# Optimization experiments

Measured on AMD Instinct MI355X. Metric: run time of the kernel, lower is better.

The kernel has to match this reference:

```python
import jax, jax.numpy as jnp
import numpy as np
from jax import lax

DIM = 128
N_CODEBOOKS = 8
CODEBOOK_SIZE = 2048
BATCH = 16
TOKENS = 2048


def setup_inputs() -> dict:
    key = jax.random.key(0)
    k1, k2 = jax.random.split(key)
    x = jax.random.normal(k1, (BATCH, DIM, TOKENS), dtype=jnp.float32)
    # matches nn.Parameter(torch.randn(K, D) / D**0.5) per stage, stacked
    codebooks = jax.random.normal(k2, (N_CODEBOOKS, CODEBOOK_SIZE, DIM),
                                  dtype=jnp.float32) / jnp.sqrt(jnp.float32(DIM))
    return {"x": x, "codebooks": codebooks}


def reference(x, codebooks):
    """Residual VQ forward.

    x: (B, D, T), codebooks: (n_cb, K, D)
    Returns (total_quantized (B,D,T), codes (B,n_cb,T) int32, commitment_loss scalar)
    """
    xt = jnp.transpose(x, (0, 2, 1))  # (B, T, D)

    def step(carry, cb):
        residual, total = carry  # (B,T,D) each; cb: (K,D)
        # squared euclidean distances: ||r||^2 - 2 r.c + ||c||^2 -> (B,T,K)
        dist = (jnp.sum(residual * residual, axis=-1, keepdims=True)
                - 2.0 * jnp.einsum('btd,kd->btk', residual, cb)
                + jnp.sum(cb * cb, axis=-1))
        idx = jnp.argmin(dist, axis=-1)          # (B, T)
        quantized = cb[idx]                       # gather -> (B, T, D)
        # straight-through combine
        q_st = residual + lax.stop_gradient(quantized - residual)
        total = total + q_st
        residual = residual - lax.stop_gradient(quantized)
        # F.mse_loss(residual.detach(), zeros) == mean(residual**2), detached
        loss = jnp.mean(lax.stop_gradient(residual) ** 2)
        return (residual, total), (idx.astype(jnp.int32), loss)

    init = (xt, jnp.zeros_like(xt))
    (_, total), (codes, losses) = lax.scan(step, init, codebooks)
    total_quantized = jnp.transpose(total, (0, 2, 1))   # (B, D, T)
    codes = jnp.transpose(codes, (1, 0, 2))             # (B, n_cb, T)
    commitment_loss = jnp.sum(losses)
    return total_quantized, codes, commitment_loss
```

## Files before the change

### kernel.cpp

```cpp
#include <hip/hip_runtime.h>

#define DIM 128
#define NCB 8
#define KSZ 2048
#define BATCH 16
#define TOK 2048
#define NTOK (BATCH * TOK)
#define NELEM (BATCH * DIM * TOK)
#define T_TILE 128
#define NTHR 512
#define CHUNK 64
#define NCHUNK (KSZ / CHUNK)

typedef float f32x4 __attribute__((ext_vector_type(4)));
typedef short s16x8 __attribute__((ext_vector_type(8)));

__device__ __forceinline__ unsigned short f2bf(float f) {
    unsigned u = __float_as_uint(f);
    u = (u + 0x7FFFu + ((u >> 16) & 1u)) >> 16;
    return (unsigned short)u;
}
__device__ __forceinline__ float bf2f(unsigned short h) {
    return __uint_as_float(((unsigned)h) << 16);
}

__global__ void rvq_prep_hi(const float* __restrict__ cbs,
                            unsigned short* __restrict__ ch) {
    int i = blockIdx.x * 256 + threadIdx.x;
    ch[i] = f2bf(cbs[i]);
}

__global__ void rvq_cnorm(const float* __restrict__ cbs,
                          float* __restrict__ cnorm,
                          float* __restrict__ loss_acc) {
    if (blockIdx.x == 0 && threadIdx.x == 0) *loss_acc = 0.0f;
    int k = blockIdx.x * 256 + threadIdx.x;
    const float4* row = (const float4*)(cbs + (size_t)k * DIM);
    float s = 0.0f;
#pragma unroll
    for (int i = 0; i < DIM / 4; ++i) {
        float4 v = row[i];
        s += v.x * v.x + v.y * v.y + v.z * v.z + v.w * v.w;
    }
    cnorm[k] = s;
}

__global__ __launch_bounds__(NTHR, 2) void rvq_fused(
        const float* __restrict__ x,
        const float* __restrict__ cbs,
        const unsigned short* __restrict__ ch,
        const float* __restrict__ cng,
        float* __restrict__ out,
        float* __restrict__ codes,
        float* __restrict__ loss_acc) {
    __shared__ float res_lds[T_TILE][DIM + 4];
    __shared__ unsigned short Bbuf[2][8192];
    __shared__ float mv1[T_TILE * 16];
    __shared__ int   mi1[T_TILE * 16];
    __shared__ float mv2[T_TILE * 16];
    __shared__ int   mi2[T_TILE * 16];
    __shared__ int   best4s[T_TILE][4];

    const int tid   = threadIdx.x;
    const int lane  = tid & 63;
    const int wv    = __builtin_amdgcn_readfirstlane(tid >> 6);
    const int col16 = lane & 15;
    const int quad  = lane >> 4;

    const int token0 = blockIdx.x * T_TILE;
    const int b      = token0 >> 11;
    const int t_in_b = token0 & (TOK - 1);

    {
        const float* xb = x + (size_t)b * DIM * TOK + t_in_b;
#pragma unroll
        for (int it = 0; it < 8; ++it) {
            int idx = it * NTHR + tid;
            int d  = idx >> 5;
            int t4 = (idx & 31) * 4;
            float4 v = *(const float4*)(xb + (size_t)d * TOK + t4);
            res_lds[t4 + 0][d] = v.x;
            res_lds[t4 + 1][d] = v.y;
            res_lds[t4 + 2][d] = v.z;
            res_lds[t4 + 3][d] = v.w;
        }
    }
    __syncthreads();

    float my_loss = 0.0f;

#define STAGE_PREFETCH(cc)                                                     \
    {                                                                          \
        int _f0 = wv * 2, _f1 = wv * 2 + 1;                                    \
        stg0 = *(const s16x8*)(ch_s +                                          \
            ((size_t)((cc) * CHUNK + (_f0 >> 2) * 16 + col16)) * DIM +         \
            ((_f0 & 3) * 32 + quad * 8));                                      \
        stg1 = *(const s16x8*)(ch_s +                                          \
            ((size_t)((cc) * CHUNK + (_f1 >> 2) * 16 + col16)) * DIM +         \
            ((_f1 & 3) * 32 + quad * 8));                                      \
    }

#define STAGE_WRITE(buf)                                                       \
    {                                                                          \
        *(s16x8*)&Bbuf[buf][(wv * 2) * 512 + lane * 8]     = stg0;             \
        *(s16x8*)&Bbuf[buf][(wv * 2 + 1) * 512 + lane * 8] = stg1;             \
    }

#define COMPUTE(accv, buf)                                                     \
    {                                                                          \
        _Pragma("unroll")                                                      \
        for (int nt = 0; nt < 4; ++nt) accv[nt] = (f32x4){0.f, 0.f, 0.f, 0.f}; \
        _Pragma("unroll")                                                      \
        for (int dc = 0; dc < 4; ++dc) {                                       \
            s16x8 bh0 = *(const s16x8*)&Bbuf[buf][(0 + dc) * 512 + lane * 8];  \
            s16x8 bh1 = *(const s16x8*)&Bbuf[buf][(4 + dc) * 512 + lane * 8];  \
            s16x8 bh2 = *(const s16x8*)&Bbuf[buf][(8 + dc) * 512 + lane * 8];  \
            s16x8 bh3 = *(const s16x8*)&Bbuf[buf][(12 + dc) * 512 + lane * 8]; \
            accv[0] = __builtin_amdgcn_mfma_f32_16x16x32_bf16(ah[dc], bh0, accv[0], 0, 0, 0); \
            accv[1] = __builtin_amdgcn_mfma_f32_16x16x32_bf16(ah[dc], bh1, accv[1], 0, 0, 0); \
            accv[2] = __builtin_amdgcn_mfma_f32_16x16x32_bf16(ah[dc], bh2, accv[2], 0, 0, 0); \
            accv[3] = __builtin_amdgcn_mfma_f32_16x16x32_bf16(ah[dc], bh3, accv[3], 0, 0, 0); \
            accv[0] = __builtin_amdgcn_mfma_f32_16x16x32_bf16(al[dc], bh0, accv[0], 0, 0, 0); \
            accv[1] = __builtin_amdgcn_mfma_f32_16x16x32_bf16(al[dc], bh1, accv[1], 0, 0, 0); \
            accv[2] = __builtin_amdgcn_mfma_f32_16x16x32_bf16(al[dc], bh2, accv[2], 0, 0, 0); \
            accv[3] = __builtin_amdgcn_mfma_f32_16x16x32_bf16(al[dc], bh3, accv[3], 0, 0, 0); \
        }                                                                      \
    }

#define FOLD(accv, cc)                                                         \
    {                                                                          \
        int _ib0 = (cc) * CHUNK + col16;                                       \
        float _cn0 = cn_s[_ib0], _cn1 = cn_s[_ib0 + 16];                       \
        float _cn2 = cn_s[_ib0 + 32], _cn3 = cn_s[_ib0 + 48];                  \
        _Pragma("unroll")                                                      \
        for (int r = 0; r < 4; ++r) {                                          \
            float p0 = fmaf(-2.0f, accv[0][r], _cn0);                          \
            float p1 = fmaf(-2.0f, accv[1][r], _cn1);                          \
            float p2 = fmaf(-2.0f, accv[2][r], _cn2);                          \
            float p3 = fmaf(-2.0f, accv[3][r], _cn3);                          \
            bool c01 = p1 < p0;                                                \
            float m01 = c01 ? p1 : p0; int j01 = c01 ? _ib0 + 16 : _ib0;       \
            bool c23 = p3 < p2;                                                \
            float m23 = c23 ? p3 : p2; int j23 = c23 ? _ib0 + 48 : _ib0 + 32;  \
            bool cf = m23 < m01;                                               \
            float m = cf ? m23 : m01; int jm = cf ? j23 : j01;                 \
            bool b1 = m < v1[r];                                               \
            bool b2 = m < v2[r];                                               \
            v2[r] = b1 ? v1[r] : (b2 ? m : v2[r]);                             \
            i2[r] = b1 ? i1[r] : (b2 ? jm : i2[r]);                            \
            v1[r] = b1 ? m : v1[r];                                            \
            i1[r] = b1 ? jm : i1[r];                                           \
        }                                                                      \
    }

#pragma unroll 1
    for (int s = 0; s < NCB; ++s) {
        const unsigned short* __restrict__ ch_s = ch  + (size_t)s * KSZ * DIM;
        const float* __restrict__ cb_s = cbs + (size_t)s * KSZ * DIM;
        const float* __restrict__ cn_s = cng + (size_t)s * KSZ;

        s16x8 ah[4], al[4];
#pragma unroll
        for (int dc = 0; dc < 4; ++dc) {
            int t  = wv * 16 + col16;
            int d0 = dc * 32 + quad * 8;
            float4 u = *(const float4*)&res_lds[t][d0];
            float4 w = *(const float4*)&res_lds[t][d0 + 4];
            float e[8] = {u.x, u.y, u.z, u.w, w.x, w.y, w.z, w.w};
            s16x8 hv, lv;
#pragma unroll
            for (int j = 0; j < 8; ++j) {
                unsigned short h = f2bf(e[j]);
                hv[j] = (short)h;
                lv[j] = (short)f2bf(e[j] - bf2f(h));
            }
            ah[dc] = hv;
            al[dc] = lv;
        }

        float v1[4], v2[4]; int i1[4], i2[4];
#pragma unroll
        for (int r = 0; r < 4; ++r) {
            v1[r] = 3.4e38f; v2[r] = 3.4e38f; i1[r] = 0; i2[r] = 0;
        }

        s16x8 stg0, stg1;
        f32x4 accA[4], accB[4];

        STAGE_PREFETCH(0); STAGE_WRITE(0); __syncthreads();
        STAGE_PREFETCH(1);
        COMPUTE(accA, 0);
        STAGE_WRITE(1); __syncthreads();
#pragma unroll 1
        for (int c = 1; c < 31; c += 2) {
            STAGE_PREFETCH(c + 1);
            COMPUTE(accB, 1);
            FOLD(accA, c - 1);
            STAGE_WRITE(0);
            __syncthreads();
            STAGE_PREFETCH(c + 2);
            COMPUTE(accA, 0);
            FOLD(accB, c);
            STAGE_WRITE(1);
            __syncthreads();
        }
        COMPUTE(accB, 1);
        FOLD(accA, 30);
        FOLD(accB, 31);

#pragma unroll
        for (int r = 0; r < 4; ++r) {
            int t = wv * 16 + quad * 4 + r;
            mv1[t * 16 + col16] = v1[r];
            mi1[t * 16 + col16] = i1[r];
            mv2[t * 16 + col16] = v2[r];
            mi2[t * 16 + col16] = i2[r];
        }
        __syncthreads();

        if (tid < T_TILE) {
            const int t = tid;
            float bv[4] = {3.4e38f, 3.4e38f, 3.4e38f, 3.4e38f};
            int   bi[4] = {0x7FFFFFFF, 0x7FFFFFFF, 0x7FFFFFFF, 0x7FFFFFFF};
#pragma unroll
            for (int col = 0; col < 16; ++col) {
#pragma unroll
                for (int w = 0; w < 2; ++w) {
                    float v = w ? mv2[t * 16 + col] : mv1[t * 16 + col];
                    int   i = w ? mi2[t * 16 + col] : mi1[t * 16 + col];
#pragma unroll
                    for (int j = 0; j < 4; ++j) {
                        if (v < bv[j] || (v == bv[j] && i < bi[j])) {
                            float tv = bv[j]; bv[j] = v; v = tv;
                            int   ti = bi[j]; bi[j] = i; i = ti;
                        }
                    }
                }
            }
#pragma unroll
            for (int j = 0; j < 4; ++j) best4s[t][j] = bi[j];
        }
        __syncthreads();

        {
            const int t  = tid >> 2;
            const int cs = tid & 3;
            const int cand = best4s[t][cs];
            const float* crow = cb_s + (size_t)cand * DIM;
            float n0 = 0, n1 = 0, n2 = 0, n3 = 0;
            float a0 = 0, a1 = 0, a2 = 0, a3 = 0;
#pragma unroll 8
            for (int d4 = 0; d4 < DIM / 4; ++d4) {
                float4 r4 = *(const float4*)&res_lds[t][d4 * 4];
                float4 q4 = *(const float4*)&crow[d4 * 4];
                n0 = fmaf(r4.x, r4.x, n0); n1 = fmaf(r4.y, r4.y, n1);
                n2 = fmaf(r4.z, r4.z, n2); n3 = fmaf(r4.w, r4.w, n3);
                a0 = fmaf(r4.x, q4.x, a0); a1 = fmaf(r4.y, q4.y, a1);
                a2 = fmaf(r4.z, q4.z, a2); a3 = fmaf(r4.w, q4.w, a3);
            }
            float rn  = (n0 + n1) + (n2 + n3);
            float dot = (a0 + a1) + (a2 + a3);
            float dist = fmaf(-2.0f, dot, rn) + cn_s[cand];
            int best = cand;
#pragma unroll
            for (int mk = 1; mk <= 2; mk <<= 1) {
                float od = __shfl_xor(dist, mk, 64);
                int   oi = __shfl_xor(best, mk, 64);
                if (od < dist || (od == dist && oi < best)) {
                    dist = od; best = oi;
                }
            }
            if (cs == 0)
                codes[(size_t)b * (NCB * TOK) + (size_t)s * TOK + t_in_b + t] =
                    (float)best;
            const float* qrow = cb_s + (size_t)best * DIM;
            float lp = 0.0f;
#pragma unroll
            for (int d4 = 0; d4 < 8; ++d4) {
                int d = cs * 32 + d4 * 4;
                float4 r4 = *(const float4*)&res_lds[t][d];
                float4 q4 = *(const float4*)&qrow[d];
                float4 nr;
                nr.x = r4.x - q4.x; nr.y = r4.y - q4.y;
                nr.z = r4.z - q4.z; nr.w = r4.w - q4.w;
                *(float4*)&res_lds[t][d] = nr;
                lp += nr.x * nr.x + nr.y * nr.y + nr.z * nr.z + nr.w * nr.w;
            }
            my_loss += lp;
        }
        __syncthreads();
    }

    {
        const float* xb = x + (size_t)b * DIM * TOK + t_in_b;
        float* ob = out + (size_t)b * DIM * TOK + t_in_b;
#pragma unroll
        for (int it = 0; it < 8; ++it) {
            int idx = it * NTHR + tid;
            int d  = idx >> 5;
            int t4 = (idx & 31) * 4;
            float4 v = *(const float4*)(xb + (size_t)d * TOK + t4);
            float4 o;
            o.x = v.x - res_lds[t4 + 0][d];
            o.y = v.y - res_lds[t4 + 1][d];
            o.z = v.z - res_lds[t4 + 2][d];
            o.w = v.w - res_lds[t4 + 3][d];
            *(float4*)(ob + (size_t)d * TOK + t4) = o;
        }
    }

#pragma unroll
    for (int off = 32; off > 0; off >>= 1)
        my_loss += __shfl_down(my_loss, off, 64);
    if (lane == 0) atomicAdd(loss_acc, my_loss);
}

__global__ void rvq_loss_fin(const float* __restrict__ loss_acc,
                             float* __restrict__ loss_out) {
    *loss_out = *loss_acc * (1.0f / (float)NELEM);
}

extern "C" void kernel_launch(void* const* d_in, const int* in_sizes, int n_in,
                              void* d_out, int out_size, void* d_ws, size_t ws_size,
                              hipStream_t stream) {
    const float* x   = (const float*)d_in[0];
    const float* cbs = (const float*)d_in[1];

    float* out      = (float*)d_out;
    float* codes    = out + NELEM;
    float* loss_out = out + NELEM + (size_t)BATCH * NCB * TOK;

    float* wsf      = (float*)d_ws;
    float* loss_acc = wsf;
    unsigned short* ch = (unsigned short*)(wsf + 256);
    float* cng = (float*)(ch + (size_t)NCB * KSZ * DIM);

    hipLaunchKernelGGL(rvq_prep_hi, dim3((NCB * KSZ * DIM) / 256), dim3(256),
                       0, stream, cbs, ch);
    hipLaunchKernelGGL(rvq_cnorm, dim3((NCB * KSZ) / 256), dim3(256), 0, stream,
                       cbs, cng, loss_acc);
    hipLaunchKernelGGL(rvq_fused, dim3(NTOK / T_TILE), dim3(NTHR), 0, stream,
                       x, cbs, ch, cng, out, codes, loss_acc);
    hipLaunchKernelGGL(rvq_loss_fin, dim3(1), dim3(1), 0, stream,
                       loss_acc, loss_out);
}
```

Measured before the change: 547.0 us.

## Halve token tile and parallelize top-4 candidate merge across threads with shuffles

Shrinks the token tile to 64 with 256 threads per block, so each wave stages four codebook fragments per chunk and the grid has twice as many blocks. The serial top-4 merge run by one thread per token is replaced by four threads per token, each merging eight candidates and then combining via xor-shuffles. This removes one barrier and the best4s LDS array. Index arrays become 16-bit and the residual row padding changes, cutting LDS use so more blocks can be resident, at the cost of re-streaming the codebook per smaller tile and possible bank-conflict changes.

```diff
diff --git a/kernel.cpp b/kernel.cpp
--- a/kernel.cpp
+++ b/kernel.cpp
@@ -7,8 +7,8 @@
 #define TOK 2048
 #define NTOK (BATCH * TOK)
 #define NELEM (BATCH * DIM * TOK)
-#define T_TILE 128
-#define NTHR 512
+#define T_TILE 64
+#define NTHR 256
 #define CHUNK 64
 #define NCHUNK (KSZ / CHUNK)
 
@@ -53,13 +53,12 @@
         float* __restrict__ out,
         float* __restrict__ codes,
         float* __restrict__ loss_acc) {
-    __shared__ float res_lds[T_TILE][DIM + 4];
+    __shared__ float res_lds[T_TILE][DIM + 2];
     __shared__ unsigned short Bbuf[2][8192];
     __shared__ float mv1[T_TILE * 16];
-    __shared__ int   mi1[T_TILE * 16];
     __shared__ float mv2[T_TILE * 16];
-    __shared__ int   mi2[T_TILE * 16];
-    __shared__ int   best4s[T_TILE][4];
+    __shared__ unsigned short mi1[T_TILE * 16];
+    __shared__ unsigned short mi2[T_TILE * 16];
 
     const int tid   = threadIdx.x;
     const int lane  = tid & 63;
@@ -76,8 +75,8 @@
 #pragma unroll
         for (int it = 0; it < 8; ++it) {
             int idx = it * NTHR + tid;
-            int d  = idx >> 5;
-            int t4 = (idx & 31) * 4;
+            int d  = idx >> 4;
+            int t4 = (idx & 15) * 4;
             float4 v = *(const float4*)(xb + (size_t)d * TOK + t4);
             res_lds[t4 + 0][d] = v.x;
             res_lds[t4 + 1][d] = v.y;
@@ -91,19 +90,20 @@
 
 #define STAGE_PREFETCH(cc)                                                     \
     {                                                                          \
-        int _f0 = wv * 2, _f1 = wv * 2 + 1;                                    \
-        stg0 = *(const s16x8*)(ch_s +                                          \
-            ((size_t)((cc) * CHUNK + (_f0 >> 2) * 16 + col16)) * DIM +         \
-            ((_f0 & 3) * 32 + quad * 8));                                      \
-        stg1 = *(const s16x8*)(ch_s +                                          \
-            ((size_t)((cc) * CHUNK + (_f1 >> 2) * 16 + col16)) * DIM +         \
-            ((_f1 & 3) * 32 + quad * 8));                                      \
+        const unsigned short* _p = ch_s +                                      \
+            ((size_t)((cc) * CHUNK + wv * 16 + col16)) * DIM + quad * 8;       \
+        stg0 = *(const s16x8*)(_p + 0);                                        \
+        stg1 = *(const s16x8*)(_p + 32);                                       \
+        stg2 = *(const s16x8*)(_p + 64);                                       \
+        stg3 = *(const s16x8*)(_p + 96);                                       \
     }
 
 #define STAGE_WRITE(buf)                                                       \
     {                                                                          \
-        *(s16x8*)&Bbuf[buf][(wv * 2) * 512 + lane * 8]     = stg0;             \
-        *(s16x8*)&Bbuf[buf][(wv * 2 + 1) * 512 + lane * 8] = stg1;             \
+        *(s16x8*)&Bbuf[buf][(wv * 4 + 0) * 512 + lane * 8] = stg0;             \
+        *(s16x8*)&Bbuf[buf][(wv * 4 + 1) * 512 + lane * 8] = stg1;             \
+        *(s16x8*)&Bbuf[buf][(wv * 4 + 2) * 512 + lane * 8] = stg2;             \
+        *(s16x8*)&Bbuf[buf][(wv * 4 + 3) * 512 + lane * 8] = stg3;             \
     }
 
 #define COMPUTE(accv, buf)                                                     \
@@ -184,7 +184,7 @@
             v1[r] = 3.4e38f; v2[r] = 3.4e38f; i1[r] = 0; i2[r] = 0;
         }
 
-        s16x8 stg0, stg1;
+        s16x8 stg0, stg1, stg2, stg3;
         f32x4 accA[4], accB[4];
 
         STAGE_PREFETCH(0); STAGE_WRITE(0); __syncthreads();
@@ -212,22 +212,47 @@
         for (int r = 0; r < 4; ++r) {
             int t = wv * 16 + quad * 4 + r;
             mv1[t * 16 + col16] = v1[r];
-            mi1[t * 16 + col16] = i1[r];
+            mi1[t * 16 + col16] = (unsigned short)i1[r];
             mv2[t * 16 + col16] = v2[r];
-            mi2[t * 16 + col16] = i2[r];
+            mi2[t * 16 + col16] = (unsigned short)i2[r];
         }
         __syncthreads();
 
-        if (tid < T_TILE) {
-            const int t = tid;
-            float bv[4] = {3.4e38f, 3.4e38f, 3.4e38f, 3.4e38f};
-            int   bi[4] = {0x7FFFFFFF, 0x7FFFFFFF, 0x7FFFFFFF, 0x7FFFFFFF};
-#pragma unroll
-            for (int col = 0; col < 16; ++col) {
-#pragma unroll
-                for (int w = 0; w < 2; ++w) {
-                    float v = w ? mv2[t * 16 + col] : mv1[t * 16 + col];
-                    int   i = w ? mi2[t * 16 + col] : mi1[t * 16 + col];
+        const int t  = tid >> 2;
+        const int cs = tid & 3;
+        float bv[4] = {3.4e38f, 3.4e38f, 3.4e38f, 3.4e38f};
+        int   bi[4] = {0x7FFFFFFF, 0x7FFFFFFF, 0x7FFFFFFF, 0x7FFFFFFF};
+        {
+            const float4 cv1 = *(const float4*)&mv1[tid * 4];
+            const float4 cv2 = *(const float4*)&mv2[tid * 4];
+            const unsigned short* ci1 = &mi1[tid * 4];
+            const unsigned short* ci2 = &mi2[tid * 4];
+            float vv[8] = {cv1.x, cv1.y, cv1.z, cv1.w,
+                           cv2.x, cv2.y, cv2.z, cv2.w};
+            int   ii[8] = {ci1[0], ci1[1], ci1[2], ci1[3],
+                           ci2[0], ci2[1], ci2[2], ci2[3]};
+#pragma unroll
+            for (int c = 0; c < 8; ++c) {
+                float v = vv[c]; int i = ii[c];
+#pragma unroll
+                for (int j = 0; j < 4; ++j) {
+                    if (v < bv[j] || (v == bv[j] && i < bi[j])) {
+                        float tv = bv[j]; bv[j] = v; v = tv;
+                        int   ti = bi[j]; bi[j] = i; i = ti;
+                    }
+                }
+            }
+#pragma unroll
+            for (int mk = 1; mk <= 2; mk <<= 1) {
+                float ov[4]; int oi[4];
+#pragma unroll
+                for (int j = 0; j < 4; ++j) {
+                    ov[j] = __shfl_xor(bv[j], mk, 64);
+                    oi[j] = __shfl_xor(bi[j], mk, 64);
+                }
+#pragma unroll
+                for (int c = 0; c < 4; ++c) {
+                    float v = ov[c]; int i = oi[c];
 #pragma unroll
                     for (int j = 0; j < 4; ++j) {
                         if (v < bv[j] || (v == bv[j] && i < bi[j])) {
@@ -237,15 +262,12 @@
                     }
                 }
             }
-#pragma unroll
-            for (int j = 0; j < 4; ++j) best4s[t][j] = bi[j];
-        }
-        __syncthreads();
+        }
+        const int cand = (cs == 0) ? bi[0]
+                       : (cs == 1) ? bi[1]
+                       : (cs == 2) ? bi[2] : bi[3];
 
         {
-            const int t  = tid >> 2;
-            const int cs = tid & 3;
-            const int cand = best4s[t][cs];
             const float* crow = cb_s + (size_t)cand * DIM;
             float n0 = 0, n1 = 0, n2 = 0, n3 = 0;
             float a0 = 0, a1 = 0, a2 = 0, a3 = 0;
@@ -297,8 +319,8 @@
 #pragma unroll
         for (int it = 0; it < 8; ++it) {
             int idx = it * NTHR + tid;
-            int d  = idx >> 5;
-            int t4 = (idx & 31) * 4;
+            int d  = idx >> 4;
+            int t4 = (idx & 15) * 4;
             float4 v = *(const float4*)(xb + (size_t)d * TOK + t4);
             float4 o;
             o.x = v.x - res_lds[t4 + 0][d];
```

Result: faster. 511.5 us (-6.5%).

## Retile MFMA waves to 32 tokens x 32 codes and parallelize top-4 merge

Applied to the files above, without the earlier changes.

Each wave now computes a 32-token by 32-code tile per chunk instead of 16 tokens by 64 codes. A-fragments are reused across two B fragments, halving LDS B reads per MFMA but doubling residual split work and running-min registers. The per-token top-4 candidate merge is spread over all 512 threads (4 per token) using shuffles, replacing the 128-thread serial loop and one barrier. Candidate indices are stored as 16-bit values to save LDS. This adds register pressure, which risks spills at the launch bound of 2 blocks.

```diff
diff --git a/kernel.cpp b/kernel.cpp
--- a/kernel.cpp
+++ b/kernel.cpp
@@ -55,17 +55,18 @@
         float* __restrict__ loss_acc) {
     __shared__ float res_lds[T_TILE][DIM + 4];
     __shared__ unsigned short Bbuf[2][8192];
-    __shared__ float mv1[T_TILE * 16];
-    __shared__ int   mi1[T_TILE * 16];
-    __shared__ float mv2[T_TILE * 16];
-    __shared__ int   mi2[T_TILE * 16];
-    __shared__ int   best4s[T_TILE][4];
+    __shared__ float mv1[T_TILE * 32];
+    __shared__ float mv2[T_TILE * 32];
+    __shared__ unsigned short mi1[T_TILE * 32];
+    __shared__ unsigned short mi2[T_TILE * 32];
 
     const int tid   = threadIdx.x;
     const int lane  = tid & 63;
     const int wv    = __builtin_amdgcn_readfirstlane(tid >> 6);
     const int col16 = lane & 15;
     const int quad  = lane >> 4;
+    const int h2    = wv & 1;
+    const int tb    = (wv >> 1) * 32;
 
     const int token0 = blockIdx.x * T_TILE;
     const int b      = token0 >> 11;
@@ -109,47 +110,42 @@
 #define COMPUTE(accv, buf)                                                     \
     {                                                                          \
         _Pragma("unroll")                                                      \
-        for (int nt = 0; nt < 4; ++nt) accv[nt] = (f32x4){0.f, 0.f, 0.f, 0.f}; \
+        for (int q = 0; q < 4; ++q) accv[q] = (f32x4){0.f, 0.f, 0.f, 0.f};     \
         _Pragma("unroll")                                                      \
         for (int dc = 0; dc < 4; ++dc) {                                       \
-            s16x8 bh0 = *(const s16x8*)&Bbuf[buf][(0 + dc) * 512 + lane * 8];  \
-            s16x8 bh1 = *(const s16x8*)&Bbuf[buf][(4 + dc) * 512 + lane * 8];  \
-            s16x8 bh2 = *(const s16x8*)&Bbuf[buf][(8 + dc) * 512 + lane * 8];  \
-            s16x8 bh3 = *(const s16x8*)&Bbuf[buf][(12 + dc) * 512 + lane * 8]; \
-            accv[0] = __builtin_amdgcn_mfma_f32_16x16x32_bf16(ah[dc], bh0, accv[0], 0, 0, 0); \
-            accv[1] = __builtin_amdgcn_mfma_f32_16x16x32_bf16(ah[dc], bh1, accv[1], 0, 0, 0); \
-            accv[2] = __builtin_amdgcn_mfma_f32_16x16x32_bf16(ah[dc], bh2, accv[2], 0, 0, 0); \
-            accv[3] = __builtin_amdgcn_mfma_f32_16x16x32_bf16(ah[dc], bh3, accv[3], 0, 0, 0); \
-            accv[0] = __builtin_amdgcn_mfma_f32_16x16x32_bf16(al[dc], bh0, accv[0], 0, 0, 0); \
-            accv[1] = __builtin_amdgcn_mfma_f32_16x16x32_bf16(al[dc], bh1, accv[1], 0, 0, 0); \
-            accv[2] = __builtin_amdgcn_mfma_f32_16x16x32_bf16(al[dc], bh2, accv[2], 0, 0, 0); \
-            accv[3] = __builtin_amdgcn_mfma_f32_16x16x32_bf16(al[dc], bh3, accv[3], 0, 0, 0); \
+            s16x8 bh0 = *(const s16x8*)&Bbuf[buf][(h2 * 8 + dc) * 512 + lane * 8];     \
+            s16x8 bh1 = *(const s16x8*)&Bbuf[buf][(h2 * 8 + 4 + dc) * 512 + lane * 8]; \
+            accv[0] = __builtin_amdgcn_mfma_f32_16x16x32_bf16(ah0[dc], bh0, accv[0], 0, 0, 0); \
+            accv[1] = __builtin_amdgcn_mfma_f32_16x16x32_bf16(ah0[dc], bh1, accv[1], 0, 0, 0); \
+            accv[2] = __builtin_amdgcn_mfma_f32_16x16x32_bf16(ah1[dc], bh0, accv[2], 0, 0, 0); \
+            accv[3] = __builtin_amdgcn_mfma_f32_16x16x32_bf16(ah1[dc], bh1, accv[3], 0, 0, 0); \
+            accv[0] = __builtin_amdgcn_mfma_f32_16x16x32_bf16(al0[dc], bh0, accv[0], 0, 0, 0); \
+            accv[1] = __builtin_amdgcn_mfma_f32_16x16x32_bf16(al0[dc], bh1, accv[1], 0, 0, 0); \
+            accv[2] = __builtin_amdgcn_mfma_f32_16x16x32_bf16(al1[dc], bh0, accv[2], 0, 0, 0); \
+            accv[3] = __builtin_amdgcn_mfma_f32_16x16x32_bf16(al1[dc], bh1, accv[3], 0, 0, 0); \
         }                                                                      \
     }
 
 #define FOLD(accv, cc)                                                         \
     {                                                                          \
-        int _ib0 = (cc) * CHUNK + col16;                                       \
+        int _ib0 = (cc) * CHUNK + h2 * 32 + col16;                             \
         float _cn0 = cn_s[_ib0], _cn1 = cn_s[_ib0 + 16];                       \
-        float _cn2 = cn_s[_ib0 + 32], _cn3 = cn_s[_ib0 + 48];                  \
         _Pragma("unroll")                                                      \
-        for (int r = 0; r < 4; ++r) {                                          \
-            float p0 = fmaf(-2.0f, accv[0][r], _cn0);                          \
-            float p1 = fmaf(-2.0f, accv[1][r], _cn1);                          \
-            float p2 = fmaf(-2.0f, accv[2][r], _cn2);                          \
-            float p3 = fmaf(-2.0f, accv[3][r], _cn3);                          \
-            bool c01 = p1 < p0;                                                \
-            float m01 = c01 ? p1 : p0; int j01 = c01 ? _ib0 + 16 : _ib0;       \
-            bool c23 = p3 < p2;                                                \
-            float m23 = c23 ? p3 : p2; int j23 = c23 ? _ib0 + 48 : _ib0 + 32;  \
-            bool cf = m23 < m01;                                               \
-            float m = cf ? m23 : m01; int jm = cf ? j23 : j01;                 \
-            bool b1 = m < v1[r];                                               \
-            bool b2 = m < v2[r];                                               \
-            v2[r] = b1 ? v1[r] : (b2 ? m : v2[r]);                             \
-            i2[r] = b1 ? i1[r] : (b2 ? jm : i2[r]);                            \
-            v1[r] = b1 ? m : v1[r];                                            \
-            i1[r] = b1 ? jm : i1[r];                                           \
+        for (int ts = 0; ts < 2; ++ts) {                                       \
+            _Pragma("unroll")                                                  \
+            for (int r = 0; r < 4; ++r) {                                      \
+                float p0 = fmaf(-2.0f, accv[ts * 2 + 0][r], _cn0);             \
+                float p1 = fmaf(-2.0f, accv[ts * 2 + 1][r], _cn1);             \
+                bool c01 = p1 < p0;                                            \
+                float m = c01 ? p1 : p0; int jm = c01 ? _ib0 + 16 : _ib0;      \
+                int vi = ts * 4 + r;                                           \
+                bool b1 = m < v1[vi];                                          \
+                bool b2 = m < v2[vi];                                          \
+                v2[vi] = b1 ? v1[vi] : (b2 ? m : v2[vi]);                      \
+                i2[vi] = b1 ? i1[vi] : (b2 ? jm : i2[vi]);                     \
+                v1[vi] = b1 ? m : v1[vi];                                      \
+                i1[vi] = b1 ? jm : i1[vi];                                     \
+            }                                                                  \
         }                                                                      \
     }
 
@@ -159,28 +155,43 @@
         const float* __restrict__ cb_s = cbs + (size_t)s * KSZ * DIM;
         const float* __restrict__ cn_s = cng + (size_t)s * KSZ;
 
-        s16x8 ah[4], al[4];
+        s16x8 ah0[4], al0[4], ah1[4], al1[4];
 #pragma unroll
         for (int dc = 0; dc < 4; ++dc) {
-            int t  = wv * 16 + col16;
             int d0 = dc * 32 + quad * 8;
-            float4 u = *(const float4*)&res_lds[t][d0];
-            float4 w = *(const float4*)&res_lds[t][d0 + 4];
-            float e[8] = {u.x, u.y, u.z, u.w, w.x, w.y, w.z, w.w};
-            s16x8 hv, lv;
-#pragma unroll
-            for (int j = 0; j < 8; ++j) {
-                unsigned short h = f2bf(e[j]);
-                hv[j] = (short)h;
-                lv[j] = (short)f2bf(e[j] - bf2f(h));
-            }
-            ah[dc] = hv;
-            al[dc] = lv;
-        }
-
-        float v1[4], v2[4]; int i1[4], i2[4];
-#pragma unroll
-        for (int r = 0; r < 4; ++r) {
+            {
+                int t = tb + col16;
+                float4 u = *(const float4*)&res_lds[t][d0];
+                float4 w = *(const float4*)&res_lds[t][d0 + 4];
+                float e[8] = {u.x, u.y, u.z, u.w, w.x, w.y, w.z, w.w};
+                s16x8 hv, lv;
+#pragma unroll
+                for (int j = 0; j < 8; ++j) {
+                    unsigned short h = f2bf(e[j]);
+                    hv[j] = (short)h;
+                    lv[j] = (short)f2bf(e[j] - bf2f(h));
+                }
+                ah0[dc] = hv; al0[dc] = lv;
+            }
+            {
+                int t = tb + 16 + col16;
+                float4 u = *(const float4*)&res_lds[t][d0];
+                float4 w = *(const float4*)&res_lds[t][d0 + 4];
+                float e[8] = {u.x, u.y, u.z, u.w, w.x, w.y, w.z, w.w};
+                s16x8 hv, lv;
+#pragma unroll
+                for (int j = 0; j < 8; ++j) {
+                    unsigned short h = f2bf(e[j]);
+                    hv[j] = (short)h;
+                    lv[j] = (short)f2bf(e[j] - bf2f(h));
+                }
+                ah1[dc] = hv; al1[dc] = lv;
+            }
+        }
+
+        float v1[8], v2[8]; int i1[8], i2[8];
+#pragma unroll
+        for (int r = 0; r < 8; ++r) {
             v1[r] = 3.4e38f; v2[r] = 3.4e38f; i1[r] = 0; i2[r] = 0;
         }
 
@@ -209,25 +220,64 @@
         FOLD(accB, 31);
 
 #pragma unroll
-        for (int r = 0; r < 4; ++r) {
-            int t = wv * 16 + quad * 4 + r;
-            mv1[t * 16 + col16] = v1[r];
-            mi1[t * 16 + col16] = i1[r];
-            mv2[t * 16 + col16] = v2[r];
-            mi2[t * 16 + col16] = i2[r];
+        for (int ts = 0; ts < 2; ++ts) {
+#pragma unroll
+            for (int r = 0; r < 4; ++r) {
+                int t = tb + ts * 16 + quad * 4 + r;
+                int o = t * 32 + h2 * 16 + col16;
+                int vi = ts * 4 + r;
+                mv1[o] = v1[vi];
+                mi1[o] = (unsigned short)i1[vi];
+                mv2[o] = v2[vi];
+                mi2[o] = (unsigned short)i2[vi];
+            }
         }
         __syncthreads();
 
-        if (tid < T_TILE) {
-            const int t = tid;
-            float bv[4] = {3.4e38f, 3.4e38f, 3.4e38f, 3.4e38f};
-            int   bi[4] = {0x7FFFFFFF, 0x7FFFFFFF, 0x7FFFFFFF, 0x7FFFFFFF};
-#pragma unroll
-            for (int col = 0; col < 16; ++col) {
-#pragma unroll
-                for (int w = 0; w < 2; ++w) {
-                    float v = w ? mv2[t * 16 + col] : mv1[t * 16 + col];
-                    int   i = w ? mi2[t * 16 + col] : mi1[t * 16 + col];
+        const int t  = tid >> 2;
+        const int cs = tid & 3;
+        float bv[4] = {3.4e38f, 3.4e38f, 3.4e38f, 3.4e38f};
+        int   bi[4] = {0x7FFFFFFF, 0x7FFFFFFF, 0x7FFFFFFF, 0x7FFFFFFF};
+        {
+            const float* MV = (cs & 2) ? mv2 : mv1;
+            const unsigned short* MI = (cs & 2) ? mi2 : mi1;
+            const int base = t * 32 + (cs & 1) * 16;
+            const float4 a0 = *(const float4*)&MV[base];
+            const float4 a1 = *(const float4*)&MV[base + 4];
+            const float4 a2 = *(const float4*)&MV[base + 8];
+            const float4 a3 = *(const float4*)&MV[base + 12];
+            const s16x8 q0 = *(const s16x8*)&MI[base];
+            const s16x8 q1 = *(const s16x8*)&MI[base + 8];
+            float vv[16] = {a0.x, a0.y, a0.z, a0.w, a1.x, a1.y, a1.z, a1.w,
+                            a2.x, a2.y, a2.z, a2.w, a3.x, a3.y, a3.z, a3.w};
+            int   ii[16];
+#pragma unroll
+            for (int j = 0; j < 8; ++j) {
+                ii[j]     = (int)(unsigned short)q0[j];
+                ii[8 + j] = (int)(unsigned short)q1[j];
+            }
+#pragma unroll
+            for (int c = 0; c < 16; ++c) {
+                float v = vv[c]; int i = ii[c];
+#pragma unroll
+                for (int j = 0; j < 4; ++j) {
+                    if (v < bv[j] || (v == bv[j] && i < bi[j])) {
+                        float tv = bv[j]; bv[j] = v; v = tv;
+                        int   ti = bi[j]; bi[j] = i; i = ti;
+                    }
+                }
+            }
+#pragma unroll
+            for (int mk = 1; mk <= 2; mk <<= 1) {
+                float ov[4]; int oi[4];
+#pragma unroll
+                for (int j = 0; j < 4; ++j) {
+                    ov[j] = __shfl_xor(bv[j], mk, 64);
+                    oi[j] = __shfl_xor(bi[j], mk, 64);
+                }
+#pragma unroll
+                for (int c = 0; c < 4; ++c) {
+                    float v = ov[c]; int i = oi[c];
 #pragma unroll
                     for (int j = 0; j < 4; ++j) {
                         if (v < bv[j] || (v == bv[j] && i < bi[j])) {
@@ -237,15 +287,12 @@
                     }
                 }
             }
-#pragma unroll
-            for (int j = 0; j < 4; ++j) best4s[t][j] = bi[j];
-        }
-        __syncthreads();
+        }
+        const int cand = (cs == 0) ? bi[0]
+                       : (cs == 1) ? bi[1]
+                       : (cs == 2) ? bi[2] : bi[3];
 
         {
-            const int t  = tid >> 2;
-            const int cs = tid & 3;
-            const int cand = best4s[t][cs];
             const float* crow = cb_s + (size_t)cand * DIM;
             float n0 = 0, n1 = 0, n2 = 0, n3 = 0;
             float a0 = 0, a1 = 0, a2 = 0, a3 = 0;
```

Result: no change. 557.7 us (+1.9%).
